# Kernel optimization log

Measured on AMD Instinct MI355X. Metric: run time of the kernel, lower is better.

## Reference

```python
import jax, jax.numpy as jnp
import numpy as np

NUM_EMBEDDINGS = 512
EMBEDDING_DIM = 64


def setup_inputs() -> dict:
    key = jax.random.key(0)
    k1, k2 = jax.random.split(key)
    z = jax.random.normal(k1, (4, EMBEDDING_DIM, 16, 64, 64), dtype=jnp.float32)
    # embedding init: uniform(-1/K, 1/K)
    bound = 1.0 / NUM_EMBEDDINGS
    emb_weight = jax.random.uniform(k2, (NUM_EMBEDDINGS, EMBEDDING_DIM),
                                    dtype=jnp.float32, minval=-bound, maxval=bound)
    return {"z": z, "emb_weight": emb_weight}


def reference(z, emb_weight):
    # z: [B, C, D, H, W] with C == embedding_dim
    B, C, D, H, W = z.shape
    z_perm = jnp.transpose(z, (0, 2, 3, 4, 1))          # [B, D, H, W, C]
    flat_z = z_perm.reshape(-1, C)                       # [N, C]
    distances = (jnp.sum(flat_z * flat_z, axis=1, keepdims=True)
                 - 2.0 * flat_z @ emb_weight.T
                 + jnp.sum(emb_weight * emb_weight, axis=1))  # [N, K]
    encoding_indices = jnp.argmin(distances, axis=1)     # [N]
    # jit-safe unique count: number of codebook entries used at least once
    counts = jnp.zeros((emb_weight.shape[0],), dtype=jnp.int32).at[encoding_indices].add(1)
    unique_codes = jnp.sum(counts > 0)
    z_q = emb_weight[encoding_indices].reshape(z_perm.shape)  # [B, D, H, W, C]
    # straight-through estimator
    z_q = z_perm + jax.lax.stop_gradient(z_q - z_perm)
    z_q = jnp.transpose(z_q, (0, 4, 1, 2, 3))            # [B, C, D, H, W]
    return z_q, unique_codes
```

## Files before the change

kernel.cpp:

```cpp
#include <hip/hip_runtime.h>

#define NPOS (4*16*64*64)
#define KCODES 512
#define CDIM 64
#define OUT_SCALAR_IDX ((size_t)NPOS * CDIM)
#define NBLK 512

#define WS_EMB   0
#define WS_EE    32768
#define WS_MASK  34816

typedef float f32x4 __attribute__((ext_vector_type(4)));
typedef long lng2 __attribute__((ext_vector_type(2)));

__global__ __launch_bounds__(64) void vq_prep(
    const float* __restrict__ emb, char* __restrict__ ws) {
  const int r = blockIdx.x * 64 + threadIdx.x;
  float c[CDIM];
  float ee = 0.f;
  #pragma unroll
  for (int q = 0; q < 16; ++q) {
    float4 x = ((const float4*)(emb + r * CDIM))[q];
    c[4*q+0] = x.x; c[4*q+1] = x.y; c[4*q+2] = x.z; c[4*q+3] = x.w;
    ee = fmaf(x.x, x.x, ee); ee = fmaf(x.y, x.y, ee);
    ee = fmaf(x.z, x.z, ee); ee = fmaf(x.w, x.w, ee);
  }
  #pragma unroll
  for (int kg = 0; kg < 4; ++kg) {
    uint u[4];
    #pragma unroll
    for (int h = 0; h < 2; ++h)
      #pragma unroll
      for (int jj = 0; jj < 2; ++jj) {
        const int kb = h * 32 + kg * 8 + jj * 4;
        uint p = __builtin_amdgcn_cvt_pk_fp8_f32(-512.f * c[kb+0], -512.f * c[kb+1], 0u, false);
        p = __builtin_amdgcn_cvt_pk_fp8_f32(-512.f * c[kb+2], -512.f * c[kb+3], p, true);
        u[h * 2 + jj] = p;
      }
    *(uint4*)(ws + WS_EMB + kg * 8192 + r * 16) = make_uint4(u[0], u[1], u[2], u[3]);
  }
  ((float*)(ws + WS_EE))[r] = 256.f * (1.f + ee);
}

__global__ __launch_bounds__(512, 4) void vq_mfma(
    const float* __restrict__ z, const float* __restrict__ emb,
    char* __restrict__ ws, float* __restrict__ out) {
  __shared__ lng2 embs[2048];
  __shared__ float s_ee[KCODES];
  __shared__ uint s_mask[16];

  const int tid = threadIdx.x;
  const int lane = tid & 63;
  const int w = tid >> 6;
  const int col = lane & 15;
  const int kg = lane >> 4;

  if (tid < 16) s_mask[tid] = 0;

  if (tid < 128)
    __builtin_amdgcn_global_load_lds(
        (const __attribute__((address_space(1))) void*)(ws + WS_EE + tid * 16),
        (__attribute__((address_space(3))) void*)((char*)s_ee + tid * 16), 16, 0, 0);
  const char* src = ws + WS_EMB;
  #pragma unroll
  for (int i = 0; i < 4; ++i) {
    const int off = (i * 512 + tid) * 16;
    __builtin_amdgcn_global_load_lds(
        (const __attribute__((address_space(1))) void*)(src + off),
        (__attribute__((address_space(3))) void*)((char*)embs + off), 16, 0, 0);
  }

  const int swz = (blockIdx.x & 7) * 64 + (blockIdx.x >> 3);
  const int nb = swz * 512;
  const int b = nb >> 16, spb = nb & 65535;
  const float* zp = z + ((size_t)b << 22) + spb + w * 64 + col;
  const int lbyte = kg * 8192 + col * 16;

  float pf0[16], pf1[16];
  long af[4][2];
  uint key[4][4];
  float4 ge[2][4];
  int gidx[2][4];

#define ISSUE(PF, RT)                                                          \
  _Pragma("unroll") for (int h = 0; h < 2; ++h)                                \
  _Pragma("unroll") for (int j = 0; j < 8; ++j)                                \
    PF[h*8+j] = zp[(RT)*16 + ((size_t)(h*32 + kg*8 + j) << 16)];

#define CONV(PF, RT)                                                           \
  {                                                                            \
    uint u0 = __builtin_amdgcn_cvt_pk_fp8_f32(PF[0], PF[1], 0u, false);        \
    u0 = __builtin_amdgcn_cvt_pk_fp8_f32(PF[2], PF[3], u0, true);              \
    uint u1 = __builtin_amdgcn_cvt_pk_fp8_f32(PF[4], PF[5], 0u, false);        \
    u1 = __builtin_amdgcn_cvt_pk_fp8_f32(PF[6], PF[7], u1, true);              \
    af[RT][0] = ((long)u1 << 32) | (long)u0;                                   \
    u0 = __builtin_amdgcn_cvt_pk_fp8_f32(PF[8], PF[9], 0u, false);             \
    u0 = __builtin_amdgcn_cvt_pk_fp8_f32(PF[10], PF[11], u0, true);            \
    u1 = __builtin_amdgcn_cvt_pk_fp8_f32(PF[12], PF[13], 0u, false);           \
    u1 = __builtin_amdgcn_cvt_pk_fp8_f32(PF[14], PF[15], u1, true);            \
    af[RT][1] = ((long)u1 << 32) | (long)u0;                                   \
  }

#define GATHER(RT, GB)                                                         \
  _Pragma("unroll") for (int s = 0; s < 4; ++s) {                              \
    const int id = (int)(((key[RT][s] >> 4) & 31u) * 16u + (key[RT][s] & 15u)); \
    gidx[GB][s] = id;                                                          \
    ge[GB][s] = ((const float4*)(emb + id * CDIM))[col];                       \
    if (col == 0) atomicOr(&s_mask[id >> 5], 1u << (id & 31));                 \
  }

#define STORE(RT, GB)                                                          \
  _Pragma("unroll") for (int s = 0; s < 4; ++s) {                              \
    float* o = out + ((size_t)b << 22) + ((size_t)(col * 4) << 16)             \
               + spb + w * 64 + (RT) * 16 + kg * 4 + s;                        \
    o[0] = ge[GB][s].x;                                                        \
    o[(size_t)1 << 16] = ge[GB][s].y;                                          \
    o[(size_t)2 << 16] = ge[GB][s].z;                                          \
    o[(size_t)3 << 16] = ge[GB][s].w;                                          \
  }

  ISSUE(pf0, 0)
  ISSUE(pf1, 1)
  CONV(pf0, 0)
  ISSUE(pf0, 2)
  CONV(pf1, 1)
  ISSUE(pf1, 3)
  CONV(pf0, 2)
  CONV(pf1, 3)

  __syncthreads();

  #pragma unroll
  for (int rt = 0; rt < 4; ++rt)
    #pragma unroll
    for (int s = 0; s < 4; ++s) key[rt][s] = 0xFFFFFFFFu;

  {
    lng2 bb = *(const lng2*)((const char*)embs + lbyte);
    float eev = s_ee[col];
    #pragma unroll 8
    for (int ct = 0; ct < 32; ++ct) {
      const lng2 bc = bb;
      const float ec = eev;
      const uint ctv = (uint)ct;
      const int nct = (ct + 1) & 31;
      bb = *(const lng2*)((const char*)embs + nct * 256 + lbyte);
      eev = s_ee[nct * 16 + col];
      const f32x4 cin = {ec, ec, ec, ec};
      #pragma unroll
      for (int rt = 0; rt < 4; ++rt) {
        f32x4 acc = __builtin_amdgcn_mfma_f32_16x16x32_fp8_fp8(af[rt][0], bc.x, cin, 0, 0, 0);
        acc = __builtin_amdgcn_mfma_f32_16x16x32_fp8_fp8(af[rt][1], bc.y, acc, 0, 0, 0);
        #pragma unroll
        for (int s = 0; s < 4; ++s) {
          uint kb = (__builtin_bit_cast(uint, acc[s]) & 0xFFFFFFE0u) | ctv;
          key[rt][s] = kb < key[rt][s] ? kb : key[rt][s];
        }
      }
    }
  }

  #pragma unroll
  for (int rt = 0; rt < 4; ++rt)
    #pragma unroll
    for (int s = 0; s < 4; ++s) {
      uint k = (key[rt][s] << 4) | (uint)col;
      #pragma unroll
      for (int m = 1; m < 16; m <<= 1) {
        uint o = (uint)__shfl_xor((int)k, m, 64);
        k = o < k ? o : k;
      }
      key[rt][s] = k;
    }

  GATHER(0, 0)
  GATHER(1, 1)
  STORE(0, 0)
  GATHER(2, 0)
  STORE(1, 1)
  GATHER(3, 1)
  STORE(2, 0)
  STORE(3, 1)

  __syncthreads();
  if (tid < 16)
    ((uint*)(ws + WS_MASK))[blockIdx.x * 16 + tid] = s_mask[tid];
}

__global__ __launch_bounds__(512) void vq_count(
    const char* __restrict__ ws, float* __restrict__ out) {
  __shared__ uint red[512];
  const int t = threadIdx.x;
  const uint* masks = (const uint*)(ws + WS_MASK);
  uint v = 0;
  #pragma unroll
  for (int g = 0; g < NBLK / 32; ++g)
    v |= masks[((t >> 4) + g * 32) * 16 + (t & 15)];
  red[t] = v;
  __syncthreads();
  for (int s = 256; s >= 16; s >>= 1) {
    if (t < s) red[t] |= red[t + s];
    __syncthreads();
  }
  if (t == 0) {
    int c = 0;
    #pragma unroll
    for (int i = 0; i < 16; ++i) c += __popc(red[i]);
    out[OUT_SCALAR_IDX] = (float)c;
  }
}

extern "C" void kernel_launch(void* const* d_in, const int* in_sizes, int n_in,
                              void* d_out, int out_size, void* d_ws, size_t ws_size,
                              hipStream_t stream) {
  const float* z = (const float*)d_in[0];
  const float* emb = (const float*)d_in[1];
  float* out = (float*)d_out;
  char* ws = (char*)d_ws;

  vq_prep<<<8, 64, 0, stream>>>(emb, ws);
  vq_mfma<<<NBLK, 512, 0, stream>>>(z, emb, ws, out);
  vq_count<<<1, 512, 0, stream>>>(ws, out);
}
```

Baseline: 37.98 us.

## Fuse codebook preprocessing into main kernel, drop separate prep launch

Removes the vq_prep kernel and has each block of the main kernel load the fp32 codebook directly, compute squared norms and fp8-convert it into LDS. Each of the 512 threads handles one code row. This removes a kernel launch and the dependency gap between launches. In exchange, every block repeats the conversion work (128KB of fp32 reads per block, mostly L2 hits) and holds 64 more registers for the row, which may raise register pressure.

```diff
diff --git a/kernel.cpp b/kernel.cpp
--- a/kernel.cpp
+++ b/kernel.cpp
@@ -6,41 +6,10 @@
 #define OUT_SCALAR_IDX ((size_t)NPOS * CDIM)
 #define NBLK 512
 
-#define WS_EMB   0
-#define WS_EE    32768
-#define WS_MASK  34816
+#define WS_MASK  0
 
 typedef float f32x4 __attribute__((ext_vector_type(4)));
 typedef long lng2 __attribute__((ext_vector_type(2)));
-
-__global__ __launch_bounds__(64) void vq_prep(
-    const float* __restrict__ emb, char* __restrict__ ws) {
-  const int r = blockIdx.x * 64 + threadIdx.x;
-  float c[CDIM];
-  float ee = 0.f;
-  #pragma unroll
-  for (int q = 0; q < 16; ++q) {
-    float4 x = ((const float4*)(emb + r * CDIM))[q];
-    c[4*q+0] = x.x; c[4*q+1] = x.y; c[4*q+2] = x.z; c[4*q+3] = x.w;
-    ee = fmaf(x.x, x.x, ee); ee = fmaf(x.y, x.y, ee);
-    ee = fmaf(x.z, x.z, ee); ee = fmaf(x.w, x.w, ee);
-  }
-  #pragma unroll
-  for (int kg = 0; kg < 4; ++kg) {
-    uint u[4];
-    #pragma unroll
-    for (int h = 0; h < 2; ++h)
-      #pragma unroll
-      for (int jj = 0; jj < 2; ++jj) {
-        const int kb = h * 32 + kg * 8 + jj * 4;
-        uint p = __builtin_amdgcn_cvt_pk_fp8_f32(-512.f * c[kb+0], -512.f * c[kb+1], 0u, false);
-        p = __builtin_amdgcn_cvt_pk_fp8_f32(-512.f * c[kb+2], -512.f * c[kb+3], p, true);
-        u[h * 2 + jj] = p;
-      }
-    *(uint4*)(ws + WS_EMB + kg * 8192 + r * 16) = make_uint4(u[0], u[1], u[2], u[3]);
-  }
-  ((float*)(ws + WS_EE))[r] = 256.f * (1.f + ee);
-}
 
 __global__ __launch_bounds__(512, 4) void vq_mfma(
     const float* __restrict__ z, const float* __restrict__ emb,
@@ -57,19 +26,6 @@
 
   if (tid < 16) s_mask[tid] = 0;
 
-  if (tid < 128)
-    __builtin_amdgcn_global_load_lds(
-        (const __attribute__((address_space(1))) void*)(ws + WS_EE + tid * 16),
-        (__attribute__((address_space(3))) void*)((char*)s_ee + tid * 16), 16, 0, 0);
-  const char* src = ws + WS_EMB;
-  #pragma unroll
-  for (int i = 0; i < 4; ++i) {
-    const int off = (i * 512 + tid) * 16;
-    __builtin_amdgcn_global_load_lds(
-        (const __attribute__((address_space(1))) void*)(src + off),
-        (__attribute__((address_space(3))) void*)((char*)embs + off), 16, 0, 0);
-  }
-
   const int swz = (blockIdx.x & 7) * 64 + (blockIdx.x >> 3);
   const int nb = swz * 512;
   const int b = nb >> 16, spb = nb & 65535;
@@ -80,7 +36,6 @@
   long af[4][2];
   uint key[4][4];
   float4 ge[2][4];
-  int gidx[2][4];
 
 #define ISSUE(PF, RT)                                                          \
   _Pragma("unroll") for (int h = 0; h < 2; ++h)                                \
@@ -104,7 +59,6 @@
 #define GATHER(RT, GB)                                                         \
   _Pragma("unroll") for (int s = 0; s < 4; ++s) {                              \
     const int id = (int)(((key[RT][s] >> 4) & 31u) * 16u + (key[RT][s] & 15u)); \
-    gidx[GB][s] = id;                                                          \
     ge[GB][s] = ((const float4*)(emb + id * CDIM))[col];                       \
     if (col == 0) atomicOr(&s_mask[id >> 5], 1u << (id & 31));                 \
   }
@@ -119,16 +73,50 @@
     o[(size_t)3 << 16] = ge[GB][s].w;                                          \
   }
 
+  float4 er[16];
+  #pragma unroll
+  for (int q = 0; q < 16; ++q)
+    er[q] = ((const float4*)(emb + tid * CDIM))[q];
+
   ISSUE(pf0, 0)
   ISSUE(pf1, 1)
+
+  {
+    float ee = 0.f;
+    #pragma unroll
+    for (int q = 0; q < 16; ++q) {
+      float4 x = er[q];
+      ee = fmaf(x.x, x.x, ee); ee = fmaf(x.y, x.y, ee);
+      ee = fmaf(x.z, x.z, ee); ee = fmaf(x.w, x.w, ee);
+    }
+    #pragma unroll
+    for (int g = 0; g < 4; ++g) {
+      uint u[4];
+      #pragma unroll
+      for (int h = 0; h < 2; ++h)
+        #pragma unroll
+        for (int jj = 0; jj < 2; ++jj) {
+          float4 x = er[(h * 32 + g * 8 + jj * 4) >> 2];
+          uint p = __builtin_amdgcn_cvt_pk_fp8_f32(-512.f * x.x, -512.f * x.y, 0u, false);
+          p = __builtin_amdgcn_cvt_pk_fp8_f32(-512.f * x.z, -512.f * x.w, p, true);
+          u[h * 2 + jj] = p;
+        }
+      *(uint4*)((char*)embs + g * 8192 + tid * 16) = make_uint4(u[0], u[1], u[2], u[3]);
+    }
+    s_ee[tid] = 256.f * (1.f + ee);
+  }
+
+  asm volatile("s_waitcnt lgkmcnt(0)" ::: "memory");
+  __builtin_amdgcn_sched_barrier(0);
+  __builtin_amdgcn_s_barrier();
+  __builtin_amdgcn_sched_barrier(0);
+
   CONV(pf0, 0)
   ISSUE(pf0, 2)
   CONV(pf1, 1)
   ISSUE(pf1, 3)
   CONV(pf0, 2)
   CONV(pf1, 3)
-
-  __syncthreads();
 
   #pragma unroll
   for (int rt = 0; rt < 4; ++rt)
@@ -218,7 +206,6 @@
   float* out = (float*)d_out;
   char* ws = (char*)d_ws;
 
-  vq_prep<<<8, 64, 0, stream>>>(emb, ws);
   vq_mfma<<<NBLK, 512, 0, stream>>>(z, emb, ws, out);
   vq_count<<<1, 512, 0, stream>>>(ws, out);
 }
```

Measured after the change: 37.74 us. No clear change (-0.6%).
